# Kernel tuning notes

Hardware: AMD Instinct MI355X
Metric: run time of the kernel (lower is better)

## Reference

```python
import jax, jax.numpy as jnp
import numpy as np

KSIZE = 3
STRIDE = 1
PADDING = 1
DILATION = 1
C_IN = 16
C_OUT = 16


def setup_inputs() -> dict:
    key = jax.random.key(0)
    k1, k2, k3 = jax.random.split(key, 3)
    inputs = jax.random.normal(k1, (2, C_IN, 24, 24, 24, 24), dtype=jnp.float32)
    weight = jax.random.normal(k2, (C_OUT, C_IN * KSIZE ** 4), dtype=jnp.float32)
    bias = jax.random.normal(k3, (1, C_OUT, 1, 1, 1, 1), dtype=jnp.float32)
    return {"inputs": inputs, "weight": weight, "bias": bias}


def reference(inputs, weight, bias):
    # weight stored flattened: [C_out, C_in * k^4] -> [C_out, C_in, k, k, k, k]
    w = weight.reshape(C_OUT, C_IN, KSIZE, KSIZE, KSIZE, KSIZE)
    # General 4-spatial-dim convolution via XLA's ND conv.
    dn = jax.lax.ConvDimensionNumbers(
        lhs_spec=(0, 1, 2, 3, 4, 5),   # N, C, U, V, H, W
        rhs_spec=(0, 1, 2, 3, 4, 5),   # O, I, kU, kV, kH, kW
        out_spec=(0, 1, 2, 3, 4, 5),
    )
    out = jax.lax.conv_general_dilated(
        inputs, w,
        window_strides=(STRIDE,) * 4,
        padding=((PADDING, PADDING),) * 4,
        rhs_dilation=(DILATION,) * 4,
        dimension_numbers=dn,
    )
    return out + bias
```

## Files before the change

### kernel.cpp

```cpp
#include <hip/hip_runtime.h>

#define S 24
#define PLANE 576
#define CISTRIDE 331776
#define SLAB_B 21632
#define QSLAB_B 6656
#define QOFF 4992
#define A_BYTES 46080
#define WS_SLABS A_BYTES

typedef __attribute__((ext_vector_type(8))) short bf16x8;
typedef __attribute__((ext_vector_type(4))) float f32x4;

__device__ __forceinline__ ushort f2bf(float f) {
    unsigned int u = __builtin_bit_cast(unsigned int, f);
    unsigned int r = u + 0x7fffu + ((u >> 16) & 1u);
    return (ushort)(r >> 16);
}

__global__ void __launch_bounds__(256)
pack_in(const float* __restrict__ in, const float* __restrict__ wgt, char* __restrict__ ws) {
    __shared__ unsigned lds_t[16][144];

    const int b = blockIdx.x;
    const int slab = b >> 1, hhp = b & 1;
    const int nb = slab / PLANE, uv = slab % PLANE;
    const float* src = in + (size_t)nb * 16 * CISTRIDE + (size_t)uv * PLANE + hhp * 288;
    char* dst = ws + WS_SLABS + (size_t)slab * SLAB_B;
    const int t = threadIdx.x;

    #pragma unroll
    for (int i = 0; i < 5; ++i) {
        int flat = i * 256 + t;
        if (flat < 1152) {
            int ci = flat / 72, q4 = flat % 72;
            float4 f = *(const float4*)(src + (size_t)ci * CISTRIDE + 4 * q4);
            uint2 pk;
            pk.x = (unsigned)f2bf(f.x) | ((unsigned)f2bf(f.y) << 16);
            pk.y = (unsigned)f2bf(f.z) | ((unsigned)f2bf(f.w) << 16);
            *(uint2*)&lds_t[ci][2 * q4] = pk;
        }
    }
    __syncthreads();

    #pragma unroll
    for (int i = 0; i < 3; ++i) {
        int c = i * 256 + t;
        if (c < 676) {
            int row_local = c / 52;
            int row = 13 * hhp + row_local;
            int cg = 676 * hhp + c;
            int pos2 = cg ^ (row & 3);
            int pos = pos2 >> 1, h = pos2 & 1;
            int col = pos - row * 26;
            uint4 o = make_uint4(0, 0, 0, 0);
            if (row >= 1 && row <= 24 && col >= 1 && col <= 24) {
                int ql = (row - 1) * 24 + (col - 1) - hhp * 288;
                int q2 = ql >> 1, odd = ql & 1;
                #pragma unroll
                for (int kk = 0; kk < 4; ++kk) {
                    unsigned a = lds_t[8 * h + 2 * kk][q2];
                    unsigned bb = lds_t[8 * h + 2 * kk + 1][q2];
                    unsigned val = odd ? ((a >> 16) | (bb & 0xffff0000u))
                                       : ((a & 0xffffu) | (bb << 16));
                    ((unsigned*)&o)[kk] = val;
                }
            }
            *(uint4*)(dst + (size_t)cg * 16) = o;
        }
    }

    if (b == 0) {
        for (int i = t; i < 2880; i += 256) {
            int step = i >> 6;
            int tap = step / 5, s = step % 5;
            int lane = i & 63;
            int co = lane & 15, gA = lane >> 4;
            int o = 2 * s + (gA >> 1);
            int cib = (gA & 1) * 8;
            ushort vals[8];
            #pragma unroll
            for (int j = 0; j < 8; ++j)
                vals[j] = (o <= 8) ? f2bf(wgt[co * 1296 + (cib + j) * 81 + tap * 9 + o]) : (ushort)0;
            uint4 pk;
            pk.x = vals[0] | ((unsigned)vals[1] << 16);
            pk.y = vals[2] | ((unsigned)vals[3] << 16);
            pk.z = vals[4] | ((unsigned)vals[5] << 16);
            pk.w = vals[6] | ((unsigned)vals[7] << 16);
            *(uint4*)(ws + (size_t)i * 16) = pk;
        }
    }
}

__global__ void __launch_bounds__(192, 4)
conv4d_main(const char* __restrict__ ws, const float* __restrict__ bias,
            float* __restrict__ out) {
    __shared__ __align__(16) char lds[2 * QSLAB_B];

    const int t = threadIdx.x, lane = t & 63, wvid = t >> 6;
    const int braw = blockIdx.x;
    const int b = (braw & 7) * 288 + (braw >> 3);
    const int nb = b / 1152, rem = b % 1152;
    const int u = rem / 48, rem2 = rem % 48;
    const int v0 = (rem2 >> 2) * 2, qq = rem2 & 3;

    const int n16 = lane & 15, g = lane >> 4;
    const int dh = n16 >> 3, dw = n16 & 7;
    const int half = g & 1, osel = g >> 1;

    int laneoff[2][5];
    #pragma unroll
    for (int trp = 0; trp < 2; ++trp)
        #pragma unroll
        for (int s = 0; s < 5; ++s) {
            int o = 2 * s + osel; if (o > 8) o = 8;
            int kh = o / 3, kw = o % 3;
            int r_off = dh + kh, c_off = dw + kw;
            int lin = (r_off * 26 + c_off) * 32 + half * 16;
            laneoff[trp][s] = lin ^ ((((trp << 1) + r_off) & 3) << 4);
        }

    f32x4 acc0[3], acc1[3];
    #pragma unroll
    for (int i = 0; i < 3; ++i) { acc0[i] = (f32x4){0,0,0,0}; acc1[i] = (f32x4){0,0,0,0}; }

    unsigned mask = 0;
    #pragma unroll
    for (int i = 0; i < 12; ++i) {
        int uu = u + (i >> 2) - 1, vv = v0 + (i & 3) - 1;
        if (uu >= 0 && uu < S && vv >= 0 && vv < S) mask |= 1u << i;
    }

    const char* slabs = ws + WS_SLABS;
    const int srcoff = qq * QOFF;
    #define SLAB_PTR(i_) (slabs + ((size_t)nb * PLANE + (u + ((i_) >> 2) - 1) * S + (v0 + ((i_) & 3) - 1)) * SLAB_B + srcoff)

    #define STAGE(bufsel_, src_) do {                                              \
        const char* _s = (src_);                                                   \
        _Pragma("unroll")                                                          \
        for (int r2 = 0; r2 < 3; ++r2) {                                           \
            int chunk = r2 * 192 + t;                                              \
            if (r2 < 2 || t < 32)                                                  \
                __builtin_amdgcn_global_load_lds(                                  \
                    (const __attribute__((address_space(1))) unsigned int*)(_s + (size_t)chunk * 16), \
                    (__attribute__((address_space(3))) unsigned int*)(lds + (bufsel_) * QSLAB_B + chunk * 16), \
                    16, 0, 0);                                                     \
        }                                                                          \
    } while (0)

    const bf16x8 zfr = {0,0,0,0,0,0,0,0};

    int cur = __ffs(mask) - 1;
    int bufsel = 0;
    STAGE(0, SLAB_PTR(cur));
    __syncthreads();

    while (1) {
        unsigned remm = mask >> (cur + 1);
        int nxt = remm ? (cur + 1 + __ffs(remm) - 1) : -1;
        if (nxt >= 0) STAGE(bufsel ^ 1, SLAB_PTR(nxt));

        const int ku = cur >> 2, dv = (cur & 3) - 1;
        const bool v0ok = dv <= 1, v1ok = dv >= 0;
        const char* ap0 = ws + (size_t)(ku * 3 + dv + 1) * 5120 + (size_t)lane * 16;
        const char* ap1 = ws + (size_t)(ku * 3 + dv) * 5120 + (size_t)lane * 16;
        bf16x8 afr0[5], afr1[5];
        #pragma unroll
        for (int s = 0; s < 5; ++s) {
            afr0[s] = v0ok ? *(const bf16x8*)(ap0 + s * 1024) : zfr;
            afr1[s] = v1ok ? *(const bf16x8*)(ap1 + s * 1024) : zfr;
        }

        const char* bp = lds + bufsel * QSLAB_B + wvid * 256;
        #pragma unroll
        for (int tr = 0; tr < 3; ++tr) {
            const int trp = (tr + qq) & 1;
            const char* bpt = bp + tr * 1664;
            #pragma unroll
            for (int s = 0; s < 5; ++s) {
                bf16x8 bfr = *(const bf16x8*)(bpt + laneoff[trp][s]);
                acc0[tr] = __builtin_amdgcn_mfma_f32_16x16x32_bf16(afr0[s], bfr, acc0[tr], 0, 0, 0);
                acc1[tr] = __builtin_amdgcn_mfma_f32_16x16x32_bf16(afr1[s], bfr, acc1[tr], 0, 0, 0);
            }
        }
        __syncthreads();
        if (nxt < 0) break;
        cur = nxt; bufsel ^= 1;
    }

    float bv[4];
    #pragma unroll
    for (int r = 0; r < 4; ++r) bv[r] = bias[g * 4 + r];
    float* outp0 = out + (size_t)nb * 16 * CISTRIDE + (size_t)(u * S + v0) * PLANE;
    float* outp1 = outp0 + PLANE;
    #pragma unroll
    for (int tr = 0; tr < 3; ++tr) {
        int row = qq * 6 + tr * 2 + dh;
        int col = wvid * 8 + dw;
        int pos = row * S + col;
        #pragma unroll
        for (int r = 0; r < 4; ++r) {
            outp0[(size_t)(g * 4 + r) * CISTRIDE + pos] = acc0[tr][r] + bv[r];
            outp1[(size_t)(g * 4 + r) * CISTRIDE + pos] = acc1[tr][r] + bv[r];
        }
    }
}

extern "C" void kernel_launch(void* const* d_in, const int* in_sizes, int n_in,
                              void* d_out, int out_size, void* d_ws, size_t ws_size,
                              hipStream_t stream) {
    const float* in   = (const float*)d_in[0];
    const float* wgt  = (const float*)d_in[1];
    const float* bias = (const float*)d_in[2];
    float* out        = (float*)d_out;
    char* ws          = (char*)d_ws;

    pack_in<<<dim3(2304), dim3(256), 0, stream>>>(in, wgt, ws);
    conv4d_main<<<dim3(2304), dim3(192), 0, stream>>>(ws, bias, out);
}
```

Baseline: 79.18 us.

## Pack whole slabs per block and issue weight loads unconditionally before staging

The packing kernel now handles a full 24x24 plane per block instead of half, batching all nine float4 loads into registers before converting and writing to LDS, and halves the grid. In the main conv kernel, the weight-fragment loads are made unconditional with clamped tap indices so they issue ahead of the next slab's async global-to-LDS staging, with a sched_barrier enforcing that order. This aims to raise memory-level parallelism in the pack and hide weight-load latency in the main loop, at the cost of more registers, a larger LDS footprint in pack, and fewer blocks.

```diff
diff --git a/kernel.cpp b/kernel.cpp
--- a/kernel.cpp
+++ b/kernel.cpp
@@ -18,45 +18,51 @@
     return (ushort)(r >> 16);
 }
 
+__device__ __forceinline__ int swz(int row, int col, int half) {
+    return (((row * 26 + col) * 32) + half * 16) ^ ((row & 3) << 4);
+}
+
 __global__ void __launch_bounds__(256)
 pack_in(const float* __restrict__ in, const float* __restrict__ wgt, char* __restrict__ ws) {
-    __shared__ unsigned lds_t[16][144];
+    __shared__ unsigned lds_t[16][288];
 
     const int b = blockIdx.x;
-    const int slab = b >> 1, hhp = b & 1;
-    const int nb = slab / PLANE, uv = slab % PLANE;
-    const float* src = in + (size_t)nb * 16 * CISTRIDE + (size_t)uv * PLANE + hhp * 288;
-    char* dst = ws + WS_SLABS + (size_t)slab * SLAB_B;
+    const int nb = b / PLANE, uv = b % PLANE;
+    const float* src = in + (size_t)nb * 16 * CISTRIDE + (size_t)uv * PLANE;
+    char* dst = ws + WS_SLABS + (size_t)b * SLAB_B;
     const int t = threadIdx.x;
 
-    #pragma unroll
-    for (int i = 0; i < 5; ++i) {
+    float4 f[9];
+    #pragma unroll
+    for (int i = 0; i < 9; ++i) {
         int flat = i * 256 + t;
-        if (flat < 1152) {
-            int ci = flat / 72, q4 = flat % 72;
-            float4 f = *(const float4*)(src + (size_t)ci * CISTRIDE + 4 * q4);
-            uint2 pk;
-            pk.x = (unsigned)f2bf(f.x) | ((unsigned)f2bf(f.y) << 16);
-            pk.y = (unsigned)f2bf(f.z) | ((unsigned)f2bf(f.w) << 16);
-            *(uint2*)&lds_t[ci][2 * q4] = pk;
-        }
+        int ci = flat / 144, q4 = flat % 144;
+        f[i] = *(const float4*)(src + (size_t)ci * CISTRIDE + 4 * q4);
+    }
+    #pragma unroll
+    for (int i = 0; i < 9; ++i) {
+        int flat = i * 256 + t;
+        int ci = flat / 144, q4 = flat % 144;
+        uint2 pk;
+        pk.x = (unsigned)f2bf(f[i].x) | ((unsigned)f2bf(f[i].y) << 16);
+        pk.y = (unsigned)f2bf(f[i].z) | ((unsigned)f2bf(f[i].w) << 16);
+        *(uint2*)&lds_t[ci][2 * q4] = pk;
     }
     __syncthreads();
 
     #pragma unroll
-    for (int i = 0; i < 3; ++i) {
+    for (int i = 0; i < 6; ++i) {
         int c = i * 256 + t;
-        if (c < 676) {
-            int row_local = c / 52;
-            int row = 13 * hhp + row_local;
-            int cg = 676 * hhp + c;
-            int pos2 = cg ^ (row & 3);
+        if (c < 1352) {
+            int k = c >> 2;
+            int row = k / 13;
+            int pos2 = c ^ (row & 3);
             int pos = pos2 >> 1, h = pos2 & 1;
             int col = pos - row * 26;
             uint4 o = make_uint4(0, 0, 0, 0);
             if (row >= 1 && row <= 24 && col >= 1 && col <= 24) {
-                int ql = (row - 1) * 24 + (col - 1) - hhp * 288;
-                int q2 = ql >> 1, odd = ql & 1;
+                int q = (row - 1) * 24 + (col - 1);
+                int q2 = q >> 1, odd = q & 1;
                 #pragma unroll
                 for (int kk = 0; kk < 4; ++kk) {
                     unsigned a = lds_t[8 * h + 2 * kk][q2];
@@ -66,7 +72,7 @@
                     ((unsigned*)&o)[kk] = val;
                 }
             }
-            *(uint4*)(dst + (size_t)cg * 16) = o;
+            *(uint4*)(dst + (size_t)c * 16) = o;
         }
     }
 
@@ -158,18 +164,24 @@
     while (1) {
         unsigned remm = mask >> (cur + 1);
         int nxt = remm ? (cur + 1 + __ffs(remm) - 1) : -1;
-        if (nxt >= 0) STAGE(bufsel ^ 1, SLAB_PTR(nxt));
 
         const int ku = cur >> 2, dv = (cur & 3) - 1;
         const bool v0ok = dv <= 1, v1ok = dv >= 0;
-        const char* ap0 = ws + (size_t)(ku * 3 + dv + 1) * 5120 + (size_t)lane * 16;
-        const char* ap1 = ws + (size_t)(ku * 3 + dv) * 5120 + (size_t)lane * 16;
+        const int t0i = min(ku * 3 + dv + 1, 8);
+        const int t1i = max(ku * 3 + dv, 0);
+        const char* ap0 = ws + (size_t)t0i * 5120 + (size_t)lane * 16;
+        const char* ap1 = ws + (size_t)t1i * 5120 + (size_t)lane * 16;
         bf16x8 afr0[5], afr1[5];
         #pragma unroll
         for (int s = 0; s < 5; ++s) {
-            afr0[s] = v0ok ? *(const bf16x8*)(ap0 + s * 1024) : zfr;
-            afr1[s] = v1ok ? *(const bf16x8*)(ap1 + s * 1024) : zfr;
-        }
+            bf16x8 r0 = *(const bf16x8*)(ap0 + s * 1024);
+            bf16x8 r1 = *(const bf16x8*)(ap1 + s * 1024);
+            afr0[s] = v0ok ? r0 : zfr;
+            afr1[s] = v1ok ? r1 : zfr;
+        }
+        __builtin_amdgcn_sched_barrier(0);
+
+        if (nxt >= 0) STAGE(bufsel ^ 1, SLAB_PTR(nxt));
 
         const char* bp = lds + bufsel * QSLAB_B + wvid * 256;
         #pragma unroll
@@ -215,6 +227,6 @@
     float* out        = (float*)d_out;
     char* ws          = (char*)d_ws;
 
-    pack_in<<<dim3(2304), dim3(256), 0, stream>>>(in, wgt, ws);
+    pack_in<<<dim3(1152), dim3(256), 0, stream>>>(in, wgt, ws);
     conv4d_main<<<dim3(2304), dim3(192), 0, stream>>>(ws, bias, out);
 }
```

Result: slower. 82.87 us (+4.7%).
